# Optimization experiments

Hardware: AMD Instinct MI355X
Metric: run time of the kernel (lower is better)

The kernel has to match this reference:

```python
import jax, jax.numpy as jnp
import numpy as np

B, T, C, H, WIN = 1, 2048, 512, 8, 48
DH = C // H  # 64


def setup_inputs() -> dict:
    key = jax.random.key(0)
    kx, kq, ko, kp = jax.random.split(key, 4)
    x = jax.random.normal(kx, (B, T, C), dtype=jnp.float32)
    W_qkv = jax.random.normal(kq, (C, 3 * C), dtype=jnp.float32) / np.sqrt(C).astype(np.float32)
    W_out = jax.random.normal(ko, (C, C), dtype=jnp.float32) / np.sqrt(C).astype(np.float32)
    # one random cycle permutation per head: perms[h, pi_pos] = original_pos
    perms = jax.vmap(lambda k: jax.random.permutation(k, T))(jax.random.split(kp, H)).astype(jnp.int32)
    return {"x": x, "W_qkv": W_qkv, "W_out": W_out, "perms": perms}


def _head_attn(qh, kh, vh, perm):
    # qh, kh, vh: [B, T, DH]; perm: [T] with perm[pi_pos] = original_pos
    Tn = perm.shape[0]
    inv_perm = jnp.argsort(perm)  # inv_perm[orig_pos] = pi_pos
    q_pi = qh[:, perm]
    k_pi = kh[:, perm]
    v_pi = vh[:, perm]
    offs = jnp.arange(-WIN, WIN + 1)                      # [W]
    pi_idx = jnp.arange(Tn)[:, None] + offs[None, :]      # [T, W]
    idx = jnp.clip(pi_idx, 0, Tn - 1)
    k_win = k_pi[:, idx]                                  # [B, T, W, DH]
    v_win = v_pi[:, idx]                                  # [B, T, W, DH]
    scores = jnp.einsum('btd,btwd->btw', q_pi, k_win) / np.sqrt(DH).astype(np.float32)
    neigh_orig = perm[idx]                                # [T, W] original positions of neighbors
    mask = (neigh_orig <= perm[:, None]) & (pi_idx >= 0) & (pi_idx < Tn)  # causal + window validity
    scores = jnp.where(mask[None], scores, jnp.finfo(scores.dtype).min)
    w = jax.nn.softmax(scores, axis=-1)                   # [B, T, W]
    y_pi = jnp.einsum('btw,btwd->btd', w, v_win)          # [B, T, DH]
    return y_pi[:, inv_perm]                              # back to original order


def reference(x, W_qkv, W_out, perms):
    qkv = x @ W_qkv                                       # [B, T, 3C]
    q, k, v = jnp.split(qkv, 3, axis=-1)
    q = q.reshape(B, T, H, DH)
    k = k.reshape(B, T, H, DH)
    v = v.reshape(B, T, H, DH)
    # heads are independent; vmap over head axis with per-head permutation
    y = jax.vmap(_head_attn, in_axes=(2, 2, 2, 0), out_axes=2)(q, k, v, perms)  # [B, T, H, DH]
    return y.reshape(B, T, C) @ W_out
```

## Files before the change

kernel.cpp:

```cpp
#include <hip/hip_runtime.h>
#include <float.h>
#include <math.h>

#define T_DIM 2048
#define C_DIM 512
#define QKV_LD 1536
#define NBLK 512
#define ATTN_SMEM 27648

typedef float f32x4 __attribute__((ext_vector_type(4)));
typedef short s16x8 __attribute__((ext_vector_type(8)));

__device__ __forceinline__ unsigned short f2bf(float f) {
  unsigned u = __float_as_uint(f);
  return (unsigned short)((u + 0x7fffu + ((u >> 16) & 1u)) >> 16);
}
__device__ __forceinline__ float bflo(unsigned u) { return __uint_as_float(u << 16); }
__device__ __forceinline__ float bfhi(unsigned u) { return __uint_as_float(u & 0xffff0000u); }

__device__ __forceinline__ void load16_to_lds(const void* g, void* l) {
  __builtin_amdgcn_global_load_lds(
      (const __attribute__((address_space(1))) unsigned int*)g,
      (__attribute__((address_space(3))) unsigned int*)(unsigned int)(unsigned long long)l,
      16, 0, 0);
}

__global__ __launch_bounds__(256) void prep_kernel(const float* __restrict__ x,
                                                   const float* __restrict__ Wqkv,
                                                   const float* __restrict__ Wout,
                                                   unsigned short* __restrict__ xbf,
                                                   unsigned short* __restrict__ WqkvT,
                                                   unsigned short* __restrict__ WoutT) {
  __shared__ float tile[32][33];
  const int tid = threadIdx.x, bid = blockIdx.x;

  const float4* xs4 = (const float4*)x;
  for (int i = bid * 256 + tid; i < (T_DIM * C_DIM) / 4; i += NBLK * 256) {
    float4 v = xs4[i];
    ushort4 o;
    o.x = f2bf(v.x); o.y = f2bf(v.y); o.z = f2bf(v.z); o.w = f2bf(v.w);
    ((ushort4*)xbf)[i] = o;
  }
  const int tx = tid & 31, ty = tid >> 5;
  for (int tt = bid; tt < 1024; tt += NBLK) {
    const float* src; unsigned short* dst; int Cc, R, bx, by;
    if (tt < 768) { src = Wqkv; dst = WqkvT; Cc = QKV_LD; R = C_DIM; bx = (tt % 48) * 32; by = (tt / 48) * 32; }
    else { int u = tt - 768; src = Wout; dst = WoutT; Cc = C_DIM; R = C_DIM; bx = (u & 15) * 32; by = (u >> 4) * 32; }
    __syncthreads();
#pragma unroll
    for (int i = 0; i < 4; ++i) { int r = ty + i * 8; tile[r][tx] = src[(size_t)(by + r) * Cc + bx + tx]; }
    __syncthreads();
#pragma unroll
    for (int i = 0; i < 4; ++i) { int r = ty + i * 8; dst[(size_t)(bx + r) * R + by + tx] = f2bf(tile[tx][r]); }
  }
}

template <int BM, int BN, bool OUT16>
__device__ __forceinline__ void gemm_body(const unsigned short* __restrict__ A,
                                          const unsigned short* __restrict__ BT,
                                          void* __restrict__ Cp,
                                          int N, int K, int tilesX,
                                          unsigned short* lA, unsigned short* lB,
                                          int tid, int bid) {
  constexpr int BK = 32;
  constexpr int BM2 = BM / 2, BN2 = BN / 2;
  constexpr int MT = BM2 / 16, NT = BN2 / 16;
  constexpr int IA = BM / 64;
  constexpr int IB = BN / 64;
  const int lane = tid & 63, w = tid >> 6, wr = w >> 1, wc = w & 1;
  const int fm = lane & 15, q8 = (lane >> 4) * 8, q4 = lane >> 4;

  const int m0 = (bid / tilesX) * BM, n0 = (bid % tilesX) * BN;
  f32x4 acc[MT][NT] = {};
  for (int k0 = 0; k0 < K; k0 += BK) {
    __syncthreads();
#pragma unroll
    for (int i = 0; i < IA; ++i) {
      int chunk = i * 256 + tid, row = chunk >> 2, c8 = (chunk & 3) * 8;
      load16_to_lds(&A[(size_t)(m0 + row) * K + k0 + c8], lA + chunk * 8);
    }
#pragma unroll
    for (int i = 0; i < IB; ++i) {
      int chunk = i * 256 + tid, row = chunk >> 2, c8 = (chunk & 3) * 8;
      load16_to_lds(&BT[(size_t)(n0 + row) * K + k0 + c8], lB + chunk * 8);
    }
    __syncthreads();
    s16x8 a[MT], b[NT];
#pragma unroll
    for (int mi = 0; mi < MT; ++mi)
      a[mi] = *(const s16x8*)&lA[(wr * BM2 + mi * 16 + fm) * BK + q8];
#pragma unroll
    for (int ni = 0; ni < NT; ++ni)
      b[ni] = *(const s16x8*)&lB[(wc * BN2 + ni * 16 + fm) * BK + q8];
#pragma unroll
    for (int mi = 0; mi < MT; ++mi)
#pragma unroll
      for (int ni = 0; ni < NT; ++ni)
        acc[mi][ni] = __builtin_amdgcn_mfma_f32_16x16x32_bf16(a[mi], b[ni], acc[mi][ni], 0, 0, 0);
  }
#pragma unroll
  for (int mi = 0; mi < MT; ++mi)
#pragma unroll
    for (int ni = 0; ni < NT; ++ni)
#pragma unroll
      for (int r = 0; r < 4; ++r) {
        int row = m0 + wr * BM2 + mi * 16 + q4 * 4 + r;
        int col = n0 + wc * BN2 + ni * 16 + fm;
        if constexpr (OUT16)
          ((unsigned short*)Cp)[(size_t)row * N + col] = f2bf(acc[mi][ni][r]);
        else
          ((float*)Cp)[(size_t)row * N + col] = acc[mi][ni][r];
      }
}

__global__ __launch_bounds__(256) void gemm1_kernel(const unsigned short* __restrict__ A,
                                                    const unsigned short* __restrict__ BT,
                                                    unsigned short* __restrict__ Cc) {
  __shared__ __align__(16) unsigned short smem[(128 + 64) * 32];
  gemm_body<128, 64, true>(A, BT, Cc, QKV_LD, C_DIM, 24, smem, smem + 128 * 32,
                           threadIdx.x, blockIdx.x);
}
__global__ __launch_bounds__(256) void gemm2_kernel(const unsigned short* __restrict__ A,
                                                    const unsigned short* __restrict__ BT,
                                                    float* __restrict__ Cc) {
  __shared__ __align__(16) unsigned short smem[(64 + 64) * 32];
  gemm_body<64, 64, false>(A, BT, Cc, C_DIM, C_DIM, 8, smem, smem + 64 * 32,
                           threadIdx.x, blockIdx.x);
}

__global__ __launch_bounds__(256) void attn_kernel(const unsigned short* __restrict__ qkvbf,
                                                   const int* __restrict__ perms,
                                                   unsigned short* __restrict__ Ybf) {
  __shared__ __align__(16) unsigned char smem[ATTN_SMEM];
  int* ow = (int*)smem;
  unsigned short* kv = (unsigned short*)(smem + 512);
  unsigned short* qb = (unsigned short*)(smem + 512 + 16384);
  unsigned short* wb = (unsigned short*)(smem + 512 + 16384 + 4096);
  const int tid = threadIdx.x, bid = blockIdx.x;
  const int lane = tid & 63, w = tid >> 6;
  const int h = bid >> 6;
  const int t0 = (bid & 63) << 5;

  if (tid < 128) {
    int pi = t0 - 48 + tid;
    int idx = min(max(pi, 0), T_DIM - 1);
    ow[tid] = perms[h * T_DIM + idx];
  }
  __syncthreads();

#pragma unroll
  for (int r = 0; r < 4; ++r) {
    int c = r * 256 + tid;
    int row = c >> 3, k = c & 7;
    uint4 d = *(const uint4*)(qkvbf + (size_t)ow[row] * QKV_LD + C_DIM + h * 64 + k * 8);
    *(uint4*)(kv + row * 64 + ((k ^ (row & 7)) * 8)) = d;
  }
  load16_to_lds(qkvbf + (size_t)ow[(tid >> 3) + 48] * QKV_LD + h * 64 + (tid & 7) * 8,
                qb + tid * 8);
  __syncthreads();

  for (int si = 0; si < 8; ++si) {
    const int s = (w << 3) + si;
    const int p = ow[s + 48];
    const int r0 = s + lane;
    const int r1 = min(r0 + 64, 127);
    const uint4* qp = (const uint4*)(qb + s * 64);
    float s0 = 0.f, s1 = 0.f;
#pragma unroll
    for (int i = 0; i < 8; ++i) {
      uint4 qv = qp[i];
      uint4 k0v = *(const uint4*)(kv + r0 * 64 + ((i ^ (r0 & 7)) * 8));
      uint4 k1v = *(const uint4*)(kv + r1 * 64 + ((i ^ (r1 & 7)) * 8));
      float q0 = bflo(qv.x), q1 = bfhi(qv.x), q2 = bflo(qv.y), q3 = bfhi(qv.y);
      float q4f = bflo(qv.z), q5 = bfhi(qv.z), q6 = bflo(qv.w), q7 = bfhi(qv.w);
      s0 += q0 * bflo(k0v.x) + q1 * bfhi(k0v.x) + q2 * bflo(k0v.y) + q3 * bfhi(k0v.y)
          + q4f * bflo(k0v.z) + q5 * bfhi(k0v.z) + q6 * bflo(k0v.w) + q7 * bfhi(k0v.w);
      s1 += q0 * bflo(k1v.x) + q1 * bfhi(k1v.x) + q2 * bflo(k1v.y) + q3 * bfhi(k1v.y)
          + q4f * bflo(k1v.z) + q5 * bfhi(k1v.z) + q6 * bflo(k1v.w) + q7 * bfhi(k1v.w);
    }
    s0 *= 0.125f; s1 *= 0.125f;
    const int pi0 = t0 - 48 + s + lane;
    const bool valid0 = (pi0 >= 0) && (pi0 < T_DIM) && (ow[r0] <= p);
    const bool valid1 = (lane < 33) && (pi0 + 64 < T_DIM) && (ow[r1] <= p);
    float mx = fmaxf(valid0 ? s0 : -FLT_MAX, valid1 ? s1 : -FLT_MAX);
#pragma unroll
    for (int off = 32; off > 0; off >>= 1) mx = fmaxf(mx, __shfl_xor(mx, off, 64));
    const float e0 = valid0 ? __expf(s0 - mx) : 0.f;
    const float e1 = valid1 ? __expf(s1 - mx) : 0.f;
    float sum = e0 + e1;
#pragma unroll
    for (int off = 32; off > 0; off >>= 1) sum += __shfl_xor(sum, off, 64);
    const float inv = 1.f / sum;
    wb[s * 104 + lane] = f2bf(e0 * inv);
    if (lane < 40) wb[s * 104 + 64 + lane] = (lane < 33) ? f2bf(e1 * inv) : (unsigned short)0;
  }
  __syncthreads();

#pragma unroll
  for (int r = 0; r < 4; ++r) {
    int c = r * 256 + tid;
    int row = c >> 3;
    load16_to_lds(qkvbf + (size_t)ow[row] * QKV_LD + 2 * C_DIM + h * 64 + (c & 7) * 8,
                  kv + c * 8);
  }
  __syncthreads();

  const int dq = lane & 15, jg = lane >> 4;
  for (int si = 0; si < 8; ++si) {
    const int s = (w << 3) + si;
    const int p = ow[s + 48];
    float4 acc = make_float4(0.f, 0.f, 0.f, 0.f);
#pragma unroll
    for (int i = 0; i < 25; ++i) {
      int j = jg + 4 * i;
      float wj = bflo((unsigned)wb[s * 104 + j]);
      uint2 vv = *(const uint2*)(kv + min(s + j, 127) * 64 + dq * 4);
      acc.x += wj * bflo(vv.x); acc.y += wj * bfhi(vv.x);
      acc.z += wj * bflo(vv.y); acc.w += wj * bfhi(vv.y);
    }
#pragma unroll
    for (int off = 16; off <= 32; off <<= 1) {
      acc.x += __shfl_xor(acc.x, off, 64);
      acc.y += __shfl_xor(acc.y, off, 64);
      acc.z += __shfl_xor(acc.z, off, 64);
      acc.w += __shfl_xor(acc.w, off, 64);
    }
    if (jg == 0) {
      ushort4 o;
      o.x = f2bf(acc.x); o.y = f2bf(acc.y); o.z = f2bf(acc.z); o.w = f2bf(acc.w);
      *(ushort4*)&Ybf[(size_t)p * C_DIM + h * 64 + dq * 4] = o;
    }
  }
}

extern "C" void kernel_launch(void* const* d_in, const int* in_sizes, int n_in,
                              void* d_out, int out_size, void* d_ws, size_t ws_size,
                              hipStream_t stream) {
  const float* x     = (const float*)d_in[0];
  const float* Wqkv  = (const float*)d_in[1];
  const float* Wout  = (const float*)d_in[2];
  const int*   perms = (const int*)d_in[3];
  float* out = (float*)d_out;
  unsigned short* ws = (unsigned short*)d_ws;

  unsigned short* xbf   = ws;
  unsigned short* WqkvT = xbf + 1048576;
  unsigned short* WoutT = WqkvT + 786432;
  unsigned short* qkvbf = WoutT + 262144;
  unsigned short* Ybf   = qkvbf + 3145728;

  prep_kernel<<<NBLK, 256, 0, stream>>>(x, Wqkv, Wout, xbf, WqkvT, WoutT);
  gemm1_kernel<<<384, 256, 0, stream>>>(xbf, WqkvT, qkvbf);
  attn_kernel<<<NBLK, 256, 0, stream>>>(qkvbf, perms, Ybf);
  gemm2_kernel<<<256, 256, 0, stream>>>(Ybf, WoutT, out);
}
```

Baseline: 112.0 us.

## Compute windowed attention scores and PV products with bf16 MFMA tiles

Replaces the scalar per-query dot products for QK^T and the weighted V sum with dense 32x128 MFMA tile products over the 128-row K/V window. Scores go to a padded LDS buffer, softmax masks to the band, and V is transposed into LDS for the second MFMA. It spends extra FLOPs on the full rectangle, and a strided transposed store of V, to cut ALU work in the attention kernel. LDS use grows, which may lower occupancy.

```diff
diff --git a/kernel.cpp b/kernel.cpp
--- a/kernel.cpp
+++ b/kernel.cpp
@@ -6,7 +6,6 @@
 #define C_DIM 512
 #define QKV_LD 1536
 #define NBLK 512
-#define ATTN_SMEM 27648
 
 typedef float f32x4 __attribute__((ext_vector_type(4)));
 typedef short s16x8 __attribute__((ext_vector_type(8)));
@@ -16,7 +15,6 @@
   return (unsigned short)((u + 0x7fffu + ((u >> 16) & 1u)) >> 16);
 }
 __device__ __forceinline__ float bflo(unsigned u) { return __uint_as_float(u << 16); }
-__device__ __forceinline__ float bfhi(unsigned u) { return __uint_as_float(u & 0xffff0000u); }
 
 __device__ __forceinline__ void load16_to_lds(const void* g, void* l) {
   __builtin_amdgcn_global_load_lds(
@@ -131,13 +129,17 @@
 __global__ __launch_bounds__(256) void attn_kernel(const unsigned short* __restrict__ qkvbf,
                                                    const int* __restrict__ perms,
                                                    unsigned short* __restrict__ Ybf) {
-  __shared__ __align__(16) unsigned char smem[ATTN_SMEM];
-  int* ow = (int*)smem;
-  unsigned short* kv = (unsigned short*)(smem + 512);
-  unsigned short* qb = (unsigned short*)(smem + 512 + 16384);
-  unsigned short* wb = (unsigned short*)(smem + 512 + 16384 + 4096);
+  __shared__ __align__(16) unsigned char smem[48768];
+  int* ow            = (int*)smem;
+  unsigned short* lQ = (unsigned short*)(smem + 512);
+  unsigned short* lK = (unsigned short*)(smem + 5120);
+  float* Sb          = (float*)(smem + 23552);
+  unsigned short* lP = (unsigned short*)(smem + 40064);
+  unsigned short* lVT= (unsigned short*)(smem + 5120);
+
   const int tid = threadIdx.x, bid = blockIdx.x;
   const int lane = tid & 63, w = tid >> 6;
+  const int fm = lane & 15, q8 = (lane >> 4) * 8, q4 = lane >> 4;
   const int h = bid >> 6;
   const int t0 = (bid & 63) << 5;
 
@@ -149,87 +151,103 @@
   __syncthreads();
 
 #pragma unroll
-  for (int r = 0; r < 4; ++r) {
-    int c = r * 256 + tid;
-    int row = c >> 3, k = c & 7;
-    uint4 d = *(const uint4*)(qkvbf + (size_t)ow[row] * QKV_LD + C_DIM + h * 64 + k * 8);
-    *(uint4*)(kv + row * 64 + ((k ^ (row & 7)) * 8)) = d;
-  }
-  load16_to_lds(qkvbf + (size_t)ow[(tid >> 3) + 48] * QKV_LD + h * 64 + (tid & 7) * 8,
-                qb + tid * 8);
-  __syncthreads();
+  for (int it = 0; it < 4; ++it) {
+    int c = it * 256 + tid;
+    int row = c >> 3, k8 = c & 7;
+    uint4 d = *(const uint4*)(qkvbf + (size_t)ow[row] * QKV_LD + C_DIM + h * 64 + k8 * 8);
+    *(uint4*)(lK + row * 72 + k8 * 8) = d;
+  }
+  {
+    int row = tid >> 3, k8 = tid & 7;
+    uint4 d = *(const uint4*)(qkvbf + (size_t)ow[48 + row] * QKV_LD + h * 64 + k8 * 8);
+    *(uint4*)(lQ + row * 72 + k8 * 8) = d;
+  }
+  __syncthreads();
+
+  {
+    f32x4 accs[2][2] = {};
+#pragma unroll
+    for (int kt = 0; kt < 2; ++kt) {
+      s16x8 aq[2];
+#pragma unroll
+      for (int mi = 0; mi < 2; ++mi)
+        aq[mi] = *(const s16x8*)&lQ[(mi * 16 + fm) * 72 + kt * 32 + q8];
+#pragma unroll
+      for (int ni = 0; ni < 2; ++ni) {
+        s16x8 bk = *(const s16x8*)&lK[(w * 32 + ni * 16 + fm) * 72 + kt * 32 + q8];
+#pragma unroll
+        for (int mi = 0; mi < 2; ++mi)
+          accs[mi][ni] = __builtin_amdgcn_mfma_f32_16x16x32_bf16(aq[mi], bk, accs[mi][ni], 0, 0, 0);
+      }
+    }
+#pragma unroll
+    for (int mi = 0; mi < 2; ++mi)
+#pragma unroll
+      for (int ni = 0; ni < 2; ++ni)
+#pragma unroll
+        for (int r = 0; r < 4; ++r)
+          Sb[(mi * 16 + q4 * 4 + r) * 129 + w * 32 + ni * 16 + fm] = accs[mi][ni][r] * 0.125f;
+  }
+  __syncthreads();
+
+#pragma unroll
+  for (int it = 0; it < 4; ++it) {
+    int c = it * 256 + tid;
+    int j = c >> 3, d0 = (c & 7) * 8;
+    uint4 v = *(const uint4*)(qkvbf + (size_t)ow[j] * QKV_LD + 2 * C_DIM + h * 64 + d0);
+    lVT[(d0 + 0) * 136 + j] = (unsigned short)(v.x & 0xffff);
+    lVT[(d0 + 1) * 136 + j] = (unsigned short)(v.x >> 16);
+    lVT[(d0 + 2) * 136 + j] = (unsigned short)(v.y & 0xffff);
+    lVT[(d0 + 3) * 136 + j] = (unsigned short)(v.y >> 16);
+    lVT[(d0 + 4) * 136 + j] = (unsigned short)(v.z & 0xffff);
+    lVT[(d0 + 5) * 136 + j] = (unsigned short)(v.z >> 16);
+    lVT[(d0 + 6) * 136 + j] = (unsigned short)(v.w & 0xffff);
+    lVT[(d0 + 7) * 136 + j] = (unsigned short)(v.w >> 16);
+  }
 
   for (int si = 0; si < 8; ++si) {
-    const int s = (w << 3) + si;
-    const int p = ow[s + 48];
-    const int r0 = s + lane;
-    const int r1 = min(r0 + 64, 127);
-    const uint4* qp = (const uint4*)(qb + s * 64);
-    float s0 = 0.f, s1 = 0.f;
-#pragma unroll
-    for (int i = 0; i < 8; ++i) {
-      uint4 qv = qp[i];
-      uint4 k0v = *(const uint4*)(kv + r0 * 64 + ((i ^ (r0 & 7)) * 8));
-      uint4 k1v = *(const uint4*)(kv + r1 * 64 + ((i ^ (r1 & 7)) * 8));
-      float q0 = bflo(qv.x), q1 = bfhi(qv.x), q2 = bflo(qv.y), q3 = bfhi(qv.y);
-      float q4f = bflo(qv.z), q5 = bfhi(qv.z), q6 = bflo(qv.w), q7 = bfhi(qv.w);
-      s0 += q0 * bflo(k0v.x) + q1 * bfhi(k0v.x) + q2 * bflo(k0v.y) + q3 * bfhi(k0v.y)
-          + q4f * bflo(k0v.z) + q5 * bfhi(k0v.z) + q6 * bflo(k0v.w) + q7 * bfhi(k0v.w);
-      s1 += q0 * bflo(k1v.x) + q1 * bfhi(k1v.x) + q2 * bflo(k1v.y) + q3 * bfhi(k1v.y)
-          + q4f * bflo(k1v.z) + q5 * bfhi(k1v.z) + q6 * bflo(k1v.w) + q7 * bfhi(k1v.w);
-    }
-    s0 *= 0.125f; s1 *= 0.125f;
-    const int pi0 = t0 - 48 + s + lane;
-    const bool valid0 = (pi0 >= 0) && (pi0 < T_DIM) && (ow[r0] <= p);
-    const bool valid1 = (lane < 33) && (pi0 + 64 < T_DIM) && (ow[r1] <= p);
-    float mx = fmaxf(valid0 ? s0 : -FLT_MAX, valid1 ? s1 : -FLT_MAX);
+    const int s = w * 8 + si;
+    const int p = ow[48 + s];
+    const int c1 = lane + 64;
+    const float v0 = Sb[s * 129 + lane];
+    const float v1 = Sb[s * 129 + c1];
+    const int pi0 = t0 - 48 + lane;
+    const bool valid0 = (lane >= s) && (pi0 >= 0) && (pi0 < T_DIM) && (ow[lane] <= p);
+    const bool valid1 = (lane <= s + 32) && (pi0 + 64 < T_DIM) && (ow[c1] <= p);
+    float mx = fmaxf(valid0 ? v0 : -FLT_MAX, valid1 ? v1 : -FLT_MAX);
 #pragma unroll
     for (int off = 32; off > 0; off >>= 1) mx = fmaxf(mx, __shfl_xor(mx, off, 64));
-    const float e0 = valid0 ? __expf(s0 - mx) : 0.f;
-    const float e1 = valid1 ? __expf(s1 - mx) : 0.f;
+    const float e0 = valid0 ? __expf(v0 - mx) : 0.f;
+    const float e1 = valid1 ? __expf(v1 - mx) : 0.f;
     float sum = e0 + e1;
 #pragma unroll
     for (int off = 32; off > 0; off >>= 1) sum += __shfl_xor(sum, off, 64);
     const float inv = 1.f / sum;
-    wb[s * 104 + lane] = f2bf(e0 * inv);
-    if (lane < 40) wb[s * 104 + 64 + lane] = (lane < 33) ? f2bf(e1 * inv) : (unsigned short)0;
-  }
-  __syncthreads();
-
-#pragma unroll
-  for (int r = 0; r < 4; ++r) {
-    int c = r * 256 + tid;
-    int row = c >> 3;
-    load16_to_lds(qkvbf + (size_t)ow[row] * QKV_LD + 2 * C_DIM + h * 64 + (c & 7) * 8,
-                  kv + c * 8);
-  }
-  __syncthreads();
-
-  const int dq = lane & 15, jg = lane >> 4;
-  for (int si = 0; si < 8; ++si) {
-    const int s = (w << 3) + si;
-    const int p = ow[s + 48];
-    float4 acc = make_float4(0.f, 0.f, 0.f, 0.f);
-#pragma unroll
-    for (int i = 0; i < 25; ++i) {
-      int j = jg + 4 * i;
-      float wj = bflo((unsigned)wb[s * 104 + j]);
-      uint2 vv = *(const uint2*)(kv + min(s + j, 127) * 64 + dq * 4);
-      acc.x += wj * bflo(vv.x); acc.y += wj * bfhi(vv.x);
-      acc.z += wj * bflo(vv.y); acc.w += wj * bfhi(vv.y);
-    }
-#pragma unroll
-    for (int off = 16; off <= 32; off <<= 1) {
-      acc.x += __shfl_xor(acc.x, off, 64);
-      acc.y += __shfl_xor(acc.y, off, 64);
-      acc.z += __shfl_xor(acc.z, off, 64);
-      acc.w += __shfl_xor(acc.w, off, 64);
-    }
-    if (jg == 0) {
-      ushort4 o;
-      o.x = f2bf(acc.x); o.y = f2bf(acc.y); o.z = f2bf(acc.z); o.w = f2bf(acc.w);
-      *(ushort4*)&Ybf[(size_t)p * C_DIM + h * 64 + dq * 4] = o;
-    }
+    lP[s * 136 + lane] = valid0 ? f2bf(e0 * inv) : (unsigned short)0;
+    lP[s * 136 + c1]   = valid1 ? f2bf(e1 * inv) : (unsigned short)0;
+  }
+  __syncthreads();
+
+  {
+    const int wr = w >> 1, wc = w & 1;
+    f32x4 acco[2] = {};
+#pragma unroll
+    for (int kt = 0; kt < 4; ++kt) {
+      s16x8 ap = *(const s16x8*)&lP[(wr * 16 + fm) * 136 + kt * 32 + q8];
+#pragma unroll
+      for (int ni = 0; ni < 2; ++ni) {
+        s16x8 bv = *(const s16x8*)&lVT[((wc * 2 + ni) * 16 + fm) * 136 + kt * 32 + q8];
+        acco[ni] = __builtin_amdgcn_mfma_f32_16x16x32_bf16(ap, bv, acco[ni], 0, 0, 0);
+      }
+    }
+#pragma unroll
+    for (int ni = 0; ni < 2; ++ni)
+#pragma unroll
+      for (int r = 0; r < 4; ++r) {
+        int q = wr * 16 + q4 * 4 + r;
+        int d = (wc * 2 + ni) * 16 + fm;
+        Ybf[(size_t)ow[48 + q] * C_DIM + h * 64 + d] = f2bf(acco[ni][r]);
+      }
   }
 }
 
```

After: 95.65 us. 1.17x faster.
